# Kernel tuning notes

Measured on AMD Instinct MI355X. Metric: run time of the kernel, lower is better.

Reference implementation:

```python
import jax, jax.numpy as jnp
import numpy as np

EPS = 1e-5

def layer_norm(x, w, b):
    mu = jnp.mean(x, axis=-1, keepdims=True)
    var = jnp.mean(jnp.square(x - mu), axis=-1, keepdims=True)
    return (x - mu) * jax.lax.rsqrt(var + EPS) * w + b

def setup_inputs() -> dict:
    key = jax.random.key(0)
    ks = jax.random.split(key, 8)
    B, T, C = 8, 512, 768
    s = 1.0 / np.sqrt(C)
    s4 = 1.0 / np.sqrt(4 * C)
    return {
        "x": jax.random.normal(ks[0], (B, T, C), dtype=jnp.float32),
        "ln1_w": jnp.ones((C,), jnp.float32),
        "ln1_b": jnp.zeros((C,), jnp.float32),
        "Wr": jax.random.normal(ks[1], (C, C), dtype=jnp.float32) * s,
        "Wk": jax.random.normal(ks[2], (C, C), dtype=jnp.float32) * s,
        "Wv": jax.random.normal(ks[3], (C, C), dtype=jnp.float32) * s,
        "time_mix_w": jnp.ones((C,), jnp.float32),  # torch init: torch.ones(n_embd)
        "Wrouter": jax.random.normal(ks[4], (C, C), dtype=jnp.float32) * s,
        "ln2_w": jnp.ones((C,), jnp.float32),
        "ln2_b": jnp.zeros((C,), jnp.float32),
        "Wck": jax.random.normal(ks[5], (4 * C, C), dtype=jnp.float32) * s,
        "Wcv": jax.random.normal(ks[6], (C, 4 * C), dtype=jnp.float32) * s4,
    }

def reference(x, ln1_w, ln1_b, Wr, Wk, Wv, time_mix_w, Wrouter, ln2_w, ln2_b, Wck, Wcv):
    B, T, C = x.shape
    xx = layer_norm(x, ln1_w, ln1_b)
    r = xx @ Wr.T
    k = xx @ Wk.T
    v = xx @ Wv.T
    w = -jnp.exp(time_mix_w)                        # (C,) negative per-channel decay rate
    idx = jnp.arange(T)
    diff = jnp.clip(idx[:, None] - idx[None, :], 0).astype(x.dtype)  # (T,T) t-j clamped at 0
    causal = jnp.tril(jnp.ones((T, T), x.dtype))
    decay = jnp.exp(w[:, None, None] * diff[None]) * causal          # (C,T,T)
    kv = k * v                                                       # (B,T,C)
    # wkv[b,t,c] = sum_j decay[c,t,j] * kv[b,j,c]
    wkv = jnp.einsum('ctj,bjc->btc', decay, kv)
    routed_wkv = wkv * jax.nn.sigmoid(xx @ Wrouter.T)
    x = x + r * routed_wkv
    xx2 = layer_norm(x, ln2_w, ln2_b)
    k_cm = jnp.square(jax.nn.relu(xx2 @ Wck.T))                      # (B,T,4C)
    return x + k_cm @ Wcv.T
```

## Files before the change

### kernel.cpp

```cpp
#include <hip/hip_runtime.h>
#include <hip/hip_bf16.h>

typedef __bf16 bf16_t;
typedef __bf16 bf16x8 __attribute__((ext_vector_type(8)));
typedef __bf16 bf16x4 __attribute__((ext_vector_type(4)));
typedef float  f32x4  __attribute__((ext_vector_type(4)));

#define LN_EPS 1e-5f


typedef __attribute__((address_space(1))) void gvoid_t;
typedef __attribute__((address_space(3))) void lvoid_t;
__device__ __forceinline__ void glds16(const void* g, void* l) {
    __builtin_amdgcn_global_load_lds((gvoid_t*)g, (lvoid_t*)l, 16, 0, 0);
}

__global__ __launch_bounds__(256) void k_cvt4(const float* __restrict__ s0,
                                              const float* __restrict__ s1,
                                              const float* __restrict__ s2,
                                              const float* __restrict__ s3,
                                              bf16_t* __restrict__ dst, int n4) {
    const float* s = (blockIdx.y == 0) ? s0 : (blockIdx.y == 1) ? s1 : (blockIdx.y == 2) ? s2 : s3;
    bf16_t* d = dst + (size_t)blockIdx.y * ((size_t)n4 * 4);
    int i = blockIdx.x * 256 + threadIdx.x;
    if (i < n4) {
        float4 v = ((const float4*)s)[i];
        bf16x4 o;
        o.x = (bf16_t)v.x; o.y = (bf16_t)v.y; o.z = (bf16_t)v.z; o.w = (bf16_t)v.w;
        ((bf16x4*)d)[i] = o;
    }
}

__global__ __launch_bounds__(256) void k_cvt2(const float* __restrict__ s0,
                                              const float* __restrict__ s1,
                                              bf16_t* __restrict__ dst, int n4) {
    const float* s = (blockIdx.y == 0) ? s0 : s1;
    bf16_t* d = dst + (size_t)blockIdx.y * ((size_t)n4 * 4);
    int i = blockIdx.x * 256 + threadIdx.x;
    if (i < n4) {
        float4 v = ((const float4*)s)[i];
        bf16x4 o;
        o.x = (bf16_t)v.x; o.y = (bf16_t)v.y; o.z = (bf16_t)v.z; o.w = (bf16_t)v.w;
        ((bf16x4*)d)[i] = o;
    }
}

__global__ __launch_bounds__(256) void k_ln(const float* __restrict__ x,
                                            const float* __restrict__ w,
                                            const float* __restrict__ b,
                                            bf16_t* __restrict__ out, int C) {
    int row = blockIdx.x;
    const float* xr = x + (long)row * C;
    int tid = threadIdx.x;
    float s = 0.f, s2 = 0.f;
    for (int i = tid; i < C; i += 256) { float v = xr[i]; s += v; s2 += v * v; }
    for (int m = 32; m; m >>= 1) { s += __shfl_xor(s, m, 64); s2 += __shfl_xor(s2, m, 64); }
    __shared__ float red[8];
    int wv = tid >> 6;
    if ((tid & 63) == 0) { red[wv] = s; red[4 + wv] = s2; }
    __syncthreads();
    float ts  = red[0] + red[1] + red[2] + red[3];
    float ts2 = red[4] + red[5] + red[6] + red[7];
    float mu  = ts / C;
    float var = ts2 / C - mu * mu;
    float rstd = rsqrtf(var + LN_EPS);
    bf16_t* orow = out + (long)row * C;
    for (int i = tid; i < C; i += 256)
        orow[i] = (bf16_t)((xr[i] - mu) * rstd * w[i] + b[i]);
}

template <int EPI, int BN>
__global__ __launch_bounds__(256) void k_gemm_bt(const bf16_t* __restrict__ A,
                                                 const bf16_t* __restrict__ Bw,
                                                 void* __restrict__ Cout,
                                                 const float* __restrict__ aux,
                                                 int N, int K, int nbn) {
    constexpr int NI = BN / 32;
    constexpr int WN = BN / 2;
    constexpr int ABUF = 128 * 32;
    constexpr int BBUF = BN * 32;
    __shared__ __align__(16) bf16_t As[2][128][32];
    __shared__ __align__(16) bf16_t Bs[2][BN][32];

    const int tid  = threadIdx.x;
    const int lane = tid & 63, wid = tid >> 6;
    const int wm = (wid >> 1) * 64, wn = (wid & 1) * WN;

    int nwg = gridDim.x;
    int cpx = nwg >> 3;
    int bid = blockIdx.x;
    int swz = (bid & 7) * cpx + (bid >> 3);
    int bm = swz / nbn, bn = swz % nbn;

    const int fr = lane & 15, ko = (lane >> 4) * 8;

    f32x4 acc[4][NI];
#pragma unroll
    for (int i = 0; i < 4; i++)
#pragma unroll
        for (int j = 0; j < NI; j++) acc[i][j] = (f32x4){0.f, 0.f, 0.f, 0.f};

    const int srow = wid * 16 + (lane >> 2);
    const int scol = (lane & 3) * 8;
    const bf16_t* Ag = A  + (size_t)(bm * 128 + srow) * K + scol;
    const bf16_t* Bg = Bw + (size_t)(bn * BN + srow) * K + scol;
    const size_t rowK64 = (size_t)64 * K;
    bf16_t* lA = &As[0][wid * 16][0];
    bf16_t* lB = &Bs[0][wid * 16][0];

#define STAGE(buf, kt)                                                          \
    do {                                                                        \
        glds16(Ag + (kt),          lA + (buf) * ABUF);                          \
        glds16(Ag + (kt) + rowK64, lA + (buf) * ABUF + 64 * 32);                \
        glds16(Bg + (kt),          lB + (buf) * BBUF);                          \
        if (BN == 128) glds16(Bg + (kt) + rowK64, lB + (buf) * BBUF + 64 * 32); \
    } while (0)

#define COMPUTE(buf)                                                                         \
    do {                                                                                     \
        bf16x8 af[4], bfr[NI];                                                               \
        _Pragma("unroll")                                                                    \
        for (int mi = 0; mi < 4; mi++) af[mi] = *(const bf16x8*)&As[buf][wm + mi * 16 + fr][ko]; \
        _Pragma("unroll")                                                                    \
        for (int ni = 0; ni < NI; ni++) bfr[ni] = *(const bf16x8*)&Bs[buf][wn + ni * 16 + fr][ko]; \
        _Pragma("unroll")                                                                    \
        for (int mi = 0; mi < 4; mi++)                                                       \
            _Pragma("unroll")                                                                \
            for (int ni = 0; ni < NI; ni++)                                                  \
                acc[mi][ni] = __builtin_amdgcn_mfma_f32_16x16x32_bf16(af[mi], bfr[ni], acc[mi][ni], 0, 0, 0); \
    } while (0)

    STAGE(0, 0);
    __syncthreads();
    int cur = 0;
    for (int kt = 0; kt < K - 32; kt += 32) {
        STAGE(cur ^ 1, kt + 32);
        COMPUTE(cur);
        __syncthreads();
        cur ^= 1;
    }
    COMPUTE(cur);

#undef STAGE
#undef COMPUTE

    const int row0 = bm * 128 + wm, col0 = bn * BN + wn;
#pragma unroll
    for (int mi = 0; mi < 4; mi++) {
#pragma unroll
        for (int ni = 0; ni < NI; ni++) {
            int row = row0 + mi * 16 + (lane >> 4) * 4;
            int col = col0 + ni * 16 + (lane & 15);
#pragma unroll
            for (int r = 0; r < 4; r++) {
                float val = acc[mi][ni][r];
                size_t off = (size_t)(row + r) * N + col;
                if (EPI == 0) {
                    ((bf16_t*)Cout)[off] = (bf16_t)val;
                } else if (EPI == 1) {
                    float t = fmaxf(val, 0.f);
                    ((bf16_t*)Cout)[off] = (bf16_t)(t * t);
                } else {
                    ((float*)Cout)[off] = aux[off] + val;
                }
            }
        }
    }
}

__global__ __launch_bounds__(256) void k_scan_local(const bf16_t* __restrict__ y4,
                                                    const float* __restrict__ tmw,
                                                    float* __restrict__ wkvl,
                                                    float* __restrict__ states) {
    int idx = blockIdx.x * 256 + threadIdx.x;
    int c   = idx % 768;
    int rem = idx / 768;
    int ch  = rem & 15;
    int b   = rem >> 4;
    float d = expf(-expf(tmw[c]));
    const bf16_t* base = y4 + ((size_t)(b * 512 + ch * 32)) * 3072 + c;
    float*        wout = wkvl + ((size_t)(b * 512 + ch * 32)) * 768 + c;
    float s = 0.f;
#pragma unroll 4
    for (int i = 0; i < 32; i++) {
        float kk = (float)base[(size_t)i * 3072 + 768];
        float vv = (float)base[(size_t)i * 3072 + 1536];
        s = s * d + kk * vv;
        wout[(size_t)i * 768] = s;
    }
    states[idx] = s;
}

__global__ __launch_bounds__(256) void k_scan_carry(const float* __restrict__ states,
                                                    const float* __restrict__ tmw,
                                                    float* __restrict__ carries) {
    int idx = blockIdx.x * 256 + threadIdx.x;
    int c = idx % 768, b = idx / 768;
    float dL = expf(-expf(tmw[c]) * 32.f);
    float s = 0.f;
    for (int ch = 0; ch < 16; ch++) {
        size_t o = ((size_t)(b * 16 + ch)) * 768 + c;
        carries[o] = s;
        s = s * dL + states[o];
    }
}

__global__ __launch_bounds__(256) void k_mix_ln(const bf16_t* __restrict__ y4,
                                                const float* __restrict__ wkvl,
                                                const float* __restrict__ carries,
                                                const float* __restrict__ tmw,
                                                const float* __restrict__ x,
                                                const float* __restrict__ w2,
                                                const float* __restrict__ b2,
                                                float* __restrict__ x1,
                                                bf16_t* __restrict__ xx2) {
    int bt = blockIdx.x;
    int t = bt & 511, b = bt >> 9;
    int tid = threadIdx.x;
    const bf16_t* yrow = y4 + (size_t)bt * 3072;
    const float*  wl   = wkvl + (size_t)bt * 768;
    const float*  cr   = carries + ((size_t)(b * 16) + (t >> 5)) * 768;
    const float*  xr   = x + (size_t)bt * 768;
    float tn = (float)((t & 31) + 1);

    float vals[3];
    float s = 0.f, s2 = 0.f;
#pragma unroll
    for (int j = 0; j < 3; j++) {
        int c = tid + j * 256;
        float rr = (float)yrow[c];
        float gg = (float)yrow[c + 2304];
        float wk = wl[c] + cr[c] * expf(-expf(tmw[c]) * tn);
        float sig = 1.f / (1.f + expf(-gg));
        float o = fmaf(rr, wk * sig, xr[c]);
        vals[j] = o; s += o; s2 += o * o;
    }
    for (int m = 32; m; m >>= 1) { s += __shfl_xor(s, m, 64); s2 += __shfl_xor(s2, m, 64); }
    __shared__ float red[8];
    int wv = tid >> 6;
    if ((tid & 63) == 0) { red[wv] = s; red[4 + wv] = s2; }
    __syncthreads();
    float ts  = red[0] + red[1] + red[2] + red[3];
    float ts2 = red[4] + red[5] + red[6] + red[7];
    float mu  = ts * (1.f / 768.f);
    float var = ts2 * (1.f / 768.f) - mu * mu;
    float rstd = rsqrtf(var + LN_EPS);
    float* x1r = x1 + (size_t)bt * 768;
    bf16_t* xo = xx2 + (size_t)bt * 768;
#pragma unroll
    for (int j = 0; j < 3; j++) {
        int c = tid + j * 256;
        x1r[c] = vals[j];
        xo[c] = (bf16_t)((vals[j] - mu) * rstd * w2[c] + b2[c]);
    }
}

extern "C" void kernel_launch(void* const* d_in, const int* in_sizes, int n_in,
                              void* d_out, int out_size, void* d_ws, size_t ws_size,
                              hipStream_t stream) {
    const float* x    = (const float*)d_in[0];
    const float* ln1w = (const float*)d_in[1];
    const float* ln1b = (const float*)d_in[2];
    const float* Wr   = (const float*)d_in[3];
    const float* Wk   = (const float*)d_in[4];
    const float* Wv   = (const float*)d_in[5];
    const float* tmw  = (const float*)d_in[6];
    const float* Wrt  = (const float*)d_in[7];
    const float* ln2w = (const float*)d_in[8];
    const float* ln2b = (const float*)d_in[9];
    const float* Wck  = (const float*)d_in[10];
    const float* Wcv  = (const float*)d_in[11];
    float* out = (float*)d_out;
    char* ws = (char*)d_ws;

    bf16_t* xx     = (bf16_t*)(ws + 0);
    bf16_t* wcat   = (bf16_t*)(ws + 6291456);
    bf16_t* wckb   = (bf16_t*)(ws + 11010048);
    bf16_t* wcvb   = (bf16_t*)(ws + 15728640);
    bf16_t* y4     = (bf16_t*)(ws + 20447232);
    bf16_t* kcm    = (bf16_t*)(ws + 20447232);
    float*  wkvl   = (float*)(ws + 70778880);
    float*  states = (float*)(ws + 83361792);
    float*  carr   = (float*)(ws + 83755008);
    float*  x1     = (float*)(ws + 84148224);

    const int n768 = 768 * 768 / 4;
    const int nbig = 3072 * 768 / 4;
    k_cvt4<<<dim3(576, 4), dim3(256), 0, stream>>>(Wr, Wk, Wv, Wrt, wcat, n768);
    k_cvt2<<<dim3(2304, 2), dim3(256), 0, stream>>>(Wck, Wcv, wckb, nbig);

    k_ln<<<dim3(4096), dim3(256), 0, stream>>>(x, ln1w, ln1b, xx, 768);

    k_gemm_bt<0, 128><<<dim3(768), dim3(256), 0, stream>>>(xx, wcat, (void*)y4, nullptr, 3072, 768, 24);

    k_scan_local<<<dim3(384), dim3(256), 0, stream>>>(y4, tmw, wkvl, states);
    k_scan_carry<<<dim3(24), dim3(256), 0, stream>>>(states, tmw, carr);
    k_mix_ln<<<dim3(4096), dim3(256), 0, stream>>>(y4, wkvl, carr, tmw, x, ln2w, ln2b, x1, xx);

    k_gemm_bt<1, 128><<<dim3(768), dim3(256), 0, stream>>>(xx, wckb, (void*)kcm, nullptr, 3072, 768, 24);

    k_gemm_bt<2, 64><<<dim3(384), dim3(256), 0, stream>>>(kcm, wcvb, (void*)out, x1, 768, 3072, 12);
}
```

Measured before the change: 158.4 us.

## Add triple-buffered GEMM pipeline, LDS swizzle, and split-K atomics for final projection

Reworks the bf16 GEMM to use three LDS buffers, with explicit vmcnt waits and barriers so global-to-LDS loads run two stages ahead of the MFMA compute. It XOR-swizzles LDS columns to reduce bank conflicts. The last GEMM (K=3072, N=768) is split along K into four 768-wide slices over 768 workgroups, accumulated with float atomicAdd into the output, which k_mix_ln now pre-initializes with the residual. This raises occupancy on the skinny GEMM but adds atomic traffic and makes the summation order nondeterministic. The loop count is hard-coded to 22 iterations, which assumes every K slice is 768.

```diff
diff --git a/kernel.cpp b/kernel.cpp
--- a/kernel.cpp
+++ b/kernel.cpp
@@ -69,86 +69,95 @@
         orow[i] = (bf16_t)((xr[i] - mu) * rstd * w[i] + b[i]);
 }
 
-template <int EPI, int BN>
+template <int EPI>
 __global__ __launch_bounds__(256) void k_gemm_bt(const bf16_t* __restrict__ A,
                                                  const bf16_t* __restrict__ Bw,
                                                  void* __restrict__ Cout,
-                                                 const float* __restrict__ aux,
-                                                 int N, int K, int nbn) {
-    constexpr int NI = BN / 32;
-    constexpr int WN = BN / 2;
-    constexpr int ABUF = 128 * 32;
-    constexpr int BBUF = BN * 32;
-    __shared__ __align__(16) bf16_t As[2][128][32];
-    __shared__ __align__(16) bf16_t Bs[2][BN][32];
-
+                                                 int N, int Ktot, int nbn, int nks) {
+    constexpr int TBUF = 128 * 32;
+    __shared__ __align__(16) bf16_t As[3][128][32];
+    __shared__ __align__(16) bf16_t Bs[3][128][32];
     const int tid  = threadIdx.x;
     const int lane = tid & 63, wid = tid >> 6;
-    const int wm = (wid >> 1) * 64, wn = (wid & 1) * WN;
+    const int wm = (wid >> 1) * 64, wn = (wid & 1) * 64;
 
     int nwg = gridDim.x;
     int cpx = nwg >> 3;
     int bid = blockIdx.x;
     int swz = (bid & 7) * cpx + (bid >> 3);
-    int bm = swz / nbn, bn = swz % nbn;
-
-    const int fr = lane & 15, ko = (lane >> 4) * 8;
-
-    f32x4 acc[4][NI];
+    int per_m = nbn * nks;
+    int bm  = swz / per_m;
+    int rem = swz % per_m;
+    int ks  = rem / nbn;
+    int bn  = rem % nbn;
+
+    const int fr = lane & 15;
+    const int swcol = ((lane >> 4) ^ (fr & 3)) * 8;
+
+    f32x4 acc[4][4];
 #pragma unroll
     for (int i = 0; i < 4; i++)
 #pragma unroll
-        for (int j = 0; j < NI; j++) acc[i][j] = (f32x4){0.f, 0.f, 0.f, 0.f};
+        for (int j = 0; j < 4; j++) acc[i][j] = (f32x4){0.f, 0.f, 0.f, 0.f};
 
     const int srow = wid * 16 + (lane >> 2);
-    const int scol = (lane & 3) * 8;
-    const bf16_t* Ag = A  + (size_t)(bm * 128 + srow) * K + scol;
-    const bf16_t* Bg = Bw + (size_t)(bn * BN + srow) * K + scol;
-    const size_t rowK64 = (size_t)64 * K;
+    const int scol = ((lane & 3) ^ ((lane >> 2) & 3)) * 8;
+    const bf16_t* Ag = A  + (size_t)(bm * 128 + srow) * Ktot + (size_t)ks * 768 + scol;
+    const bf16_t* Bg = Bw + (size_t)(bn * 128 + srow) * Ktot + (size_t)ks * 768 + scol;
+    const size_t rowK64 = (size_t)64 * Ktot;
     bf16_t* lA = &As[0][wid * 16][0];
     bf16_t* lB = &Bs[0][wid * 16][0];
 
-#define STAGE(buf, kt)                                                          \
-    do {                                                                        \
-        glds16(Ag + (kt),          lA + (buf) * ABUF);                          \
-        glds16(Ag + (kt) + rowK64, lA + (buf) * ABUF + 64 * 32);                \
-        glds16(Bg + (kt),          lB + (buf) * BBUF);                          \
-        if (BN == 128) glds16(Bg + (kt) + rowK64, lB + (buf) * BBUF + 64 * 32); \
+#define STAGE(buf, kt)                                              \
+    do {                                                            \
+        glds16(Ag + (kt),          lA + (buf) * TBUF);              \
+        glds16(Ag + (kt) + rowK64, lA + (buf) * TBUF + 64 * 32);    \
+        glds16(Bg + (kt),          lB + (buf) * TBUF);              \
+        glds16(Bg + (kt) + rowK64, lB + (buf) * TBUF + 64 * 32);    \
     } while (0)
 
 #define COMPUTE(buf)                                                                         \
     do {                                                                                     \
-        bf16x8 af[4], bfr[NI];                                                               \
+        bf16x8 af[4], bfr[4];                                                                \
         _Pragma("unroll")                                                                    \
-        for (int mi = 0; mi < 4; mi++) af[mi] = *(const bf16x8*)&As[buf][wm + mi * 16 + fr][ko]; \
+        for (int mi = 0; mi < 4; mi++) af[mi] = *(const bf16x8*)&As[buf][wm + mi * 16 + fr][swcol]; \
         _Pragma("unroll")                                                                    \
-        for (int ni = 0; ni < NI; ni++) bfr[ni] = *(const bf16x8*)&Bs[buf][wn + ni * 16 + fr][ko]; \
+        for (int ni = 0; ni < 4; ni++) bfr[ni] = *(const bf16x8*)&Bs[buf][wn + ni * 16 + fr][swcol]; \
         _Pragma("unroll")                                                                    \
         for (int mi = 0; mi < 4; mi++)                                                       \
             _Pragma("unroll")                                                                \
-            for (int ni = 0; ni < NI; ni++)                                                  \
+            for (int ni = 0; ni < 4; ni++)                                                   \
                 acc[mi][ni] = __builtin_amdgcn_mfma_f32_16x16x32_bf16(af[mi], bfr[ni], acc[mi][ni], 0, 0, 0); \
     } while (0)
 
     STAGE(0, 0);
-    __syncthreads();
-    int cur = 0;
-    for (int kt = 0; kt < K - 32; kt += 32) {
-        STAGE(cur ^ 1, kt + 32);
-        COMPUTE(cur);
-        __syncthreads();
-        cur ^= 1;
-    }
-    COMPUTE(cur);
+    STAGE(1, 32);
+    int ba = 0, bb = 1, bc = 2;
+    for (int it = 0; it < 22; ++it) {
+        asm volatile("s_waitcnt vmcnt(4)" ::: "memory");
+        __builtin_amdgcn_s_barrier();
+        __builtin_amdgcn_sched_barrier(0);
+        STAGE(bc, (it + 2) * 32);
+        COMPUTE(ba);
+        int t = ba; ba = bb; bb = bc; bc = t;
+    }
+    asm volatile("s_waitcnt vmcnt(4)" ::: "memory");
+    __builtin_amdgcn_s_barrier();
+    __builtin_amdgcn_sched_barrier(0);
+    COMPUTE(ba);
+    asm volatile("s_waitcnt vmcnt(0)" ::: "memory");
+    __builtin_amdgcn_s_barrier();
+    __builtin_amdgcn_sched_barrier(0);
+    COMPUTE(bb);
 
 #undef STAGE
 #undef COMPUTE
 
-    const int row0 = bm * 128 + wm, col0 = bn * BN + wn;
+    const int row0 = bm * 128 + wm, col0 = bn * 128 + wn;
 #pragma unroll
     for (int mi = 0; mi < 4; mi++) {
 #pragma unroll
-        for (int ni = 0; ni < NI; ni++) {
+        for (int ni = 0; ni < 4; ni++) {
             int row = row0 + mi * 16 + (lane >> 4) * 4;
             int col = col0 + ni * 16 + (lane & 15);
 #pragma unroll
@@ -161,7 +170,7 @@
                     float t = fmaxf(val, 0.f);
                     ((bf16_t*)Cout)[off] = (bf16_t)(t * t);
                 } else {
-                    ((float*)Cout)[off] = aux[off] + val;
+                    atomicAdd(&((float*)Cout)[off], val);
                 }
             }
         }
@@ -212,7 +221,7 @@
                                                 const float* __restrict__ x,
                                                 const float* __restrict__ w2,
                                                 const float* __restrict__ b2,
-                                                float* __restrict__ x1,
+                                                float* __restrict__ out,
                                                 bf16_t* __restrict__ xx2) {
     int bt = blockIdx.x;
     int t = bt & 511, b = bt >> 9;
@@ -245,12 +254,12 @@
     float mu  = ts * (1.f / 768.f);
     float var = ts2 * (1.f / 768.f) - mu * mu;
     float rstd = rsqrtf(var + LN_EPS);
-    float* x1r = x1 + (size_t)bt * 768;
+    float* orow = out + (size_t)bt * 768;
     bf16_t* xo = xx2 + (size_t)bt * 768;
 #pragma unroll
     for (int j = 0; j < 3; j++) {
         int c = tid + j * 256;
-        x1r[c] = vals[j];
+        orow[c] = vals[j];
         xo[c] = (bf16_t)((vals[j] - mu) * rstd * w2[c] + b2[c]);
     }
 }
@@ -282,7 +291,6 @@
     float*  wkvl   = (float*)(ws + 70778880);
     float*  states = (float*)(ws + 83361792);
     float*  carr   = (float*)(ws + 83755008);
-    float*  x1     = (float*)(ws + 84148224);
 
     const int n768 = 768 * 768 / 4;
     const int nbig = 3072 * 768 / 4;
@@ -291,13 +299,13 @@
 
     k_ln<<<dim3(4096), dim3(256), 0, stream>>>(x, ln1w, ln1b, xx, 768);
 
-    k_gemm_bt<0, 128><<<dim3(768), dim3(256), 0, stream>>>(xx, wcat, (void*)y4, nullptr, 3072, 768, 24);
+    k_gemm_bt<0><<<dim3(768), dim3(256), 0, stream>>>(xx, wcat, (void*)y4, 3072, 768, 24, 1);
 
     k_scan_local<<<dim3(384), dim3(256), 0, stream>>>(y4, tmw, wkvl, states);
     k_scan_carry<<<dim3(24), dim3(256), 0, stream>>>(states, tmw, carr);
-    k_mix_ln<<<dim3(4096), dim3(256), 0, stream>>>(y4, wkvl, carr, tmw, x, ln2w, ln2b, x1, xx);
-
-    k_gemm_bt<1, 128><<<dim3(768), dim3(256), 0, stream>>>(xx, wckb, (void*)kcm, nullptr, 3072, 768, 24);
-
-    k_gemm_bt<2, 64><<<dim3(384), dim3(256), 0, stream>>>(kcm, wcvb, (void*)out, x1, 768, 3072, 12);
-}
+    k_mix_ln<<<dim3(4096), dim3(256), 0, stream>>>(y4, wkvl, carr, tmw, x, ln2w, ln2b, out, xx);
+
+    k_gemm_bt<1><<<dim3(768), dim3(256), 0, stream>>>(xx, wckb, (void*)kcm, 3072, 768, 24, 1);
+
+    k_gemm_bt<3><<<dim3(768), dim3(256), 0, stream>>>(kcm, wcvb, (void*)out, 768, 3072, 6, 4);
+}
```

Result: slower. 163.5 us (+3.2%).
